# Performance work log

Measured on AMD Instinct MI355X. Metric: run time of the kernel, lower is better.

The kernel has to match this reference:

```python
import jax, jax.numpy as jnp
import numpy as np


def open_uniform_knots(n_ctrl: int, p: int):
    # open-uniform knot vector on [0, 1]: n_ctrl + p + 1 knots
    interior = np.linspace(0.0, 1.0, n_ctrl - p + 1)[1:-1]
    return jnp.asarray(
        np.concatenate([np.zeros(p + 1), interior, np.ones(p + 1)]), jnp.float32
    )


def bspline_basis_1d(u, knots, p: int, n_ctrl: int):
    """Cox-de Boor (NURBS book A2.2), vectorized over queries.
    Returns (N [Q, p+1] nonzero basis values, span [Q] knot-span index)."""
    span = jnp.clip(jnp.searchsorted(knots, u, side='right') - 1, p, n_ctrl - 1)
    left = jnp.stack([u - knots[span + 1 - j] for j in range(1, p + 1)], axis=-1)
    right = jnp.stack([knots[span + j] - u for j in range(1, p + 1)], axis=-1)
    N = [jnp.ones_like(u)]
    for j in range(1, p + 1):
        saved = jnp.zeros_like(u)
        Nn = []
        for r in range(j):
            temp = N[r] / (right[..., r] + left[..., j - 1 - r])
            Nn.append(saved + right[..., r] * temp)
            saved = left[..., j - 1 - r] * temp
        Nn.append(saved)
        N = Nn
    return jnp.stack(N, axis=-1), span


def setup_inputs() -> dict:
    key = jax.random.key(0)
    kq, kc = jax.random.split(key)
    n_points, dim_in = 2_000_000, 3
    n_ctrl, degree, dim_out = 32, 3, 3
    queries = jax.random.uniform(kq, (n_points, dim_in), dtype=jnp.float32)
    control_points = jax.random.normal(kc, (n_ctrl ** 3, dim_out), dtype=jnp.float32)
    return {"queries": queries, "control_points": control_points,
            "degree": degree, "n_ctrl": n_ctrl}


def reference(queries, control_points, degree, n_ctrl):
    p, n = int(degree), int(n_ctrl)
    knots = open_uniform_knots(n, p)
    # per-dim nonzero basis values and spans
    Bx, sx = bspline_basis_1d(queries[:, 0], knots, p, n)
    By, sy = bspline_basis_1d(queries[:, 1], knots, p, n)
    Bz, sz = bspline_basis_1d(queries[:, 2], knots, p, n)
    offs = jnp.arange(p + 1)
    ix = sx[:, None] - p + offs  # [Q, p+1] local control-point indices (x fastest)
    iy = sy[:, None] - p + offs
    iz = sz[:, None] - p + offs
    Q, d = queries.shape[0], control_points.shape[1]
    out = jnp.zeros((Q, d), control_points.dtype)
    # sparse local-support combine: only (p+1)^3 control points per query,
    # looped over the two outer local axes (fixed small loop), gathered on x
    for k in range(p + 1):
        for j in range(p + 1):
            flat = ix + n * (iy[:, j:j + 1] + n * iz[:, k:k + 1])  # [Q, p+1]
            Cg = control_points[flat]  # [Q, p+1, d]
            w = Bz[:, k] * By[:, j]  # [Q]
            out = out + w[:, None] * jnp.einsum('qi,qid->qd', Bx, Cg)
    return out
```

## Files before the change

kernel.cpp:

```cpp
#include <hip/hip_runtime.h>


#define NCTRL 32
#define NSEG 29
#define SCALE (5.5f / 127.0f)
#define INV_SCALE (127.0f / 5.5f)

typedef unsigned int u32x4 __attribute__((ext_vector_type(4)));
typedef _Float16 h2 __attribute__((ext_vector_type(2)));
using native_h2 = decltype(__builtin_amdgcn_cvt_pkrtz(0.0f, 0.0f));

__device__ __forceinline__ h2 pkrtz(float a, float b) {
    return __builtin_bit_cast(h2, __builtin_amdgcn_cvt_pkrtz(a, b));
}
__device__ __forceinline__ float fdot2f(h2 a, h2 b, float c) {
    return __builtin_amdgcn_fdot2(__builtin_bit_cast(native_h2, a),
                                  __builtin_bit_cast(native_h2, b), c, false);
}
__device__ __forceinline__ h2 permh(unsigned int d, unsigned int sel) {
    return __builtin_bit_cast(h2, __builtin_amdgcn_perm(0x64646464u, d, sel));
}

__device__ __forceinline__ void basis_w(float U, float ft, float N[4]) {
    float x  = U - ft;
    float r1 = 1.0f - x;
    float km1 = fmaxf(ft - 1.0f, 0.0f);
    float km2 = fmaxf(ft - 2.0f, 0.0f);
    float kp2 = fminf(ft + 2.0f, (float)NSEG);
    float kp3 = fminf(ft + 3.0f, (float)NSEG);
    float l2 = U - km1, l3 = U - km2;
    float r2 = kp2 - U, r3 = kp3 - U;
    float N0 = r1, N1 = x;
    float rcp20 = __builtin_amdgcn_rcpf(ft + 1.0f - km1);
    float rcp21 = __builtin_amdgcn_rcpf(kp2 - ft);
    float temp  = N0 * rcp20;
    N0 = r1 * temp;
    float saved = l2 * temp;
    temp = N1 * rcp21;
    N1 = saved + r2 * temp;
    float N2 = x * temp;
    float rcp30 = __builtin_amdgcn_rcpf(ft + 1.0f - km2);
    float rcp31 = __builtin_amdgcn_rcpf(kp2 - km1);
    float rcp32 = __builtin_amdgcn_rcpf(kp3 - ft);
    temp = N0 * rcp30;
    N0 = r1 * temp;
    saved = l3 * temp;
    temp = N1 * rcp31;
    N1 = saved + r2 * temp;
    saved = l2 * temp;
    temp = N2 * rcp32;
    N2 = saved + r3 * temp;
    N[0] = N0; N[1] = N1; N[2] = N2; N[3] = x * temp;
}

__device__ __forceinline__ unsigned char quant8(float v) {
    float b = fminf(fmaxf(rintf(v * INV_SCALE) + 128.0f, 0.0f), 255.0f);
    return (unsigned char)(int)b;
}

__global__ void __launch_bounds__(256) repack_q8v2(const float* __restrict__ cp,
                                                   unsigned char* __restrict__ tabA,
                                                   unsigned char* __restrict__ tabB,
                                                   int nA, int nTot) {
    int i4 = blockIdx.x * blockDim.x + threadIdx.x;
    int ib = i4 * 4;
    if (ib >= nTot) return;
    unsigned int w;
    unsigned int* dst;
    if (ib < nA) {
        int beta = ib & 63, L = ib >> 6;
        int x0 = L % NSEG;
        int t2 = L / NSEG;
        int yw = t2 % NSEG;
        int zb = t2 / NSEG;
        int c = beta >> 4, j = (beta & 15) >> 2;
        int s = (zb * NCTRL + (yw + j)) * NCTRL + (x0 + c);
        unsigned int b0 = quant8(cp[3 * s + 0]);
        unsigned int b1 = quant8(cp[3 * s + 1]);
        unsigned int b2 = quant8(cp[3 * (s + NCTRL * NCTRL) + 0]);
        unsigned int b3 = quant8(cp[3 * (s + NCTRL * NCTRL) + 1]);
        w = b0 | (b1 << 8) | (b2 << 16) | (b3 << 24);
        dst = (unsigned int*)(tabA + ib);
    } else {
        int ii = ib - nA;
        int beta = ii & 63, L = ii >> 6;
        int x0 = L % NSEG;
        int t2 = L / NSEG;
        int yw = t2 % NSEG;
        int zw = t2 / NSEG;
        int c = beta >> 4, j = (beta & 15) >> 2;
        int s = (zw * NCTRL + (yw + j)) * NCTRL + (x0 + c);
        unsigned int b0 = quant8(cp[3 * (s + 0 * NCTRL * NCTRL) + 2]);
        unsigned int b1 = quant8(cp[3 * (s + 1 * NCTRL * NCTRL) + 2]);
        unsigned int b2 = quant8(cp[3 * (s + 2 * NCTRL * NCTRL) + 2]);
        unsigned int b3 = quant8(cp[3 * (s + 3 * NCTRL * NCTRL) + 2]);
        w = b0 | (b1 << 8) | (b2 << 16) | (b3 << 24);
        dst = (unsigned int*)(tabB + ii);
    }
    *dst = w;
}


#define LINE_STRIDE 1040
#define BUF_LDS (4 * LINE_STRIDE)
#define WAVE_LDS (2 * BUF_LDS)

__device__ __forceinline__ void stage16(const unsigned char* src,
                                        unsigned char* dst_wave_uniform) {
    __builtin_amdgcn_global_load_lds(
        (const __attribute__((address_space(1))) void*)src,
        (__attribute__((address_space(3))) void*)dst_wave_uniform, 16, 0, 0);
}

__global__ void __launch_bounds__(128, 4) spline_eval_q8v7(const float* __restrict__ q,
                                                           const unsigned char* __restrict__ tabA,
                                                           const unsigned char* __restrict__ tabB,
                                                           float* __restrict__ out, int Q) {
    __shared__ unsigned char smem[2 * WAVE_LDS];
    int t = blockIdx.x * blockDim.x + threadIdx.x;
    bool valid = t < Q;
    int g = valid ? t : (Q - 1);
    int lane = threadIdx.x & 63;
    unsigned char* wbase = &smem[(threadIdx.x >> 6) * WAVE_LDS];
    unsigned char* b0 = wbase;
    unsigned char* b1 = wbase + BUF_LDS;

    int bidx = lane & 60;
    unsigned sub16 = (((unsigned)(lane & 3) - (unsigned)(lane >> 3)) & 3u) << 4;
    const unsigned char* lb0 =
        b0 + (lane >> 4) * LINE_STRIDE + (lane & 15) * 64;
    const unsigned char* lb1 = lb0 + BUF_LDS;
    unsigned t16 = ((unsigned)((lane & 15) >> 1) & 3u) << 4;
    const u32x4* a0p[4];
    const u32x4* a1p[4];
#pragma unroll
    for (int x = 0; x < 4; ++x) {
        unsigned co = (t16 + (unsigned)x * 16u) & 48u;
        a0p[x] = (const u32x4*)(lb0 + co);
        a1p[x] = (const u32x4*)(lb1 + co);
    }
    const unsigned char* pA1 = tabA + 107648u;

    float3 qv = *(const float3*)(q + 3 * (size_t)g);
    float Ux = qv.x * (float)NSEG, Uy = qv.y * (float)NSEG, Uz = qv.z * (float)NSEG;
    float fx = fminf(fmaxf(floorf(Ux), 0.0f), (float)(NSEG - 1));
    float fy = fminf(fmaxf(floorf(Uy), 0.0f), (float)(NSEG - 1));
    float fz = fminf(fmaxf(floorf(Uz), 0.0f), (float)(NSEG - 1));
    int sx = (int)fx, sy = (int)fy, sz = (int)fz;
    int L = (sz * NSEG + sy) * NSEG + sx;

    unsigned voff[4];
#pragma unroll
    for (int grp = 0; grp < 4; ++grp) {
        int Lg = __builtin_amdgcn_ds_bpermute((grp << 6) + bidx, L);
        voff[grp] = ((unsigned)Lg << 6) + sub16;
    }

#pragma unroll
    for (int grp = 0; grp < 4; ++grp)
        stage16(tabA + voff[grp], b0 + grp * LINE_STRIDE);
#pragma unroll
    for (int grp = 0; grp < 4; ++grp)
        stage16(pA1 + voff[grp], b1 + grp * LINE_STRIDE);

    float Bx[4], By[4], Bz[4];
    basis_w(Ux, fx, Bx);
    basis_w(Uy, fy, By);
    basis_w(Uz, fz, Bz);

    h2 Bz01 = pkrtz(Bz[0], Bz[1]);
    h2 Bz23 = pkrtz(Bz[2], Bz[3]);
    const h2 one2 = {(_Float16)1.0f, (_Float16)1.0f};
    h2 wpk[4][2];
    float sumw = 0.0f;
#pragma unroll
    for (int j = 0; j < 4; ++j) {
        h2 Byj = pkrtz(By[j], By[j]);
        wpk[j][0] = Byj * Bz01;
        wpk[j][1] = Byj * Bz23;
        sumw = fdot2f(wpk[j][0], one2, sumw);
        sumw = fdot2f(wpk[j][1], one2, sumw);
    }

    u32x4 c0[4], c1[4];

    asm volatile("s_waitcnt vmcnt(4)" ::: "memory");
#pragma unroll
    for (int x = 0; x < 4; ++x) c0[x] = *a0p[x];
    asm volatile("s_waitcnt vmcnt(0)" ::: "memory");
#pragma unroll
    for (int x = 0; x < 4; ++x) c1[x] = *a1p[x];
    asm volatile("s_waitcnt lgkmcnt(0)" ::: "memory");
    __builtin_amdgcn_sched_barrier(0);
#pragma unroll
    for (int grp = 0; grp < 4; ++grp)
        stage16(tabB + voff[grp], b0 + grp * LINE_STRIDE);

    float axs[4], ays[4];
#pragma unroll
    for (int x = 0; x < 4; ++x) {
        float ax = 0.0f, ay = 0.0f;
#pragma unroll
        for (int j = 0; j < 4; ++j) {
            unsigned d = c0[x][j];
            ax = fdot2f(permh(d, 0x04020400u), wpk[j][0], ax);
            ay = fdot2f(permh(d, 0x04030401u), wpk[j][0], ay);
        }
        axs[x] = ax; ays[x] = ay;
    }
#pragma unroll
    for (int x = 0; x < 4; ++x) {
        float ax = axs[x], ay = ays[x];
#pragma unroll
        for (int j = 0; j < 4; ++j) {
            unsigned d = c1[x][j];
            ax = fdot2f(permh(d, 0x04020400u), wpk[j][1], ax);
            ay = fdot2f(permh(d, 0x04030401u), wpk[j][1], ay);
        }
        axs[x] = ax; ays[x] = ay;
    }

    asm volatile("s_waitcnt vmcnt(0)" ::: "memory");
#pragma unroll
    for (int x = 0; x < 4; ++x) c0[x] = *a0p[x];
    float vx = 0.0f, vy = 0.0f;
#pragma unroll
    for (int x = 0; x < 4; ++x) {
        vx = fmaf(Bx[x], axs[x], vx);
        vy = fmaf(Bx[x], ays[x], vy);
    }
    float mb = (-1152.0f * SCALE) * sumw;
    vx = fmaf(vx, SCALE, mb);
    vy = fmaf(vy, SCALE, mb);

    float vz = 0.0f;
#pragma unroll
    for (int x = 0; x < 4; ++x) {
        float az = 0.0f;
#pragma unroll
        for (int j = 0; j < 4; ++j) {
            unsigned d = c0[x][j];
            az = fdot2f(permh(d, 0x04010400u), wpk[j][0], az);
            az = fdot2f(permh(d, 0x04030402u), wpk[j][1], az);
        }
        vz = fmaf(Bx[x], az, vz);
    }
    vz = fmaf(vz, SCALE, mb);

    if (valid) {
        float3 o; o.x = vx; o.y = vy; o.z = vz;
        *(float3*)(out + 3 * (size_t)g) = o;
    }
}

__global__ void __launch_bounds__(256) spline_eval_direct(const float* __restrict__ q,
                                                          const float* __restrict__ cp,
                                                          float* __restrict__ out, int Q) {
    int idx = blockIdx.x * blockDim.x + threadIdx.x;
    if (idx >= Q) return;
    float U[3], ft[3];
    int s[3];
#pragma unroll
    for (int d = 0; d < 3; ++d) {
        U[d]  = q[3 * idx + d] * (float)NSEG;
        ft[d] = fminf(fmaxf(floorf(U[d]), 0.0f), (float)(NSEG - 1));
        s[d]  = (int)ft[d];
    }
    float Bx[4], By[4], Bz[4];
    basis_w(U[0], ft[0], Bx);
    basis_w(U[1], ft[1], By);
    basis_w(U[2], ft[2], Bz);
    float ax = 0.f, ay = 0.f, az = 0.f;
#pragma unroll
    for (int k = 0; k < 4; ++k) {
#pragma unroll
        for (int j = 0; j < 4; ++j) {
            float w = Bz[k] * By[j];
            int base = ((s[2] + k) * NCTRL + (s[1] + j)) * NCTRL + s[0];
#pragma unroll
            for (int i = 0; i < 4; ++i) {
                float wi = w * Bx[i];
                ax = fmaf(wi, cp[3 * (base + i) + 0], ax);
                ay = fmaf(wi, cp[3 * (base + i) + 1], ay);
                az = fmaf(wi, cp[3 * (base + i) + 2], az);
            }
        }
    }
    out[3 * idx + 0] = ax;
    out[3 * idx + 1] = ay;
    out[3 * idx + 2] = az;
}

extern "C" void kernel_launch(void* const* d_in, const int* in_sizes, int n_in,
                              void* d_out, int out_size, void* d_ws, size_t ws_size,
                              hipStream_t stream) {
    const float* q  = (const float*)d_in[0];
    const float* cp = (const float*)d_in[1];
    float* out = (float*)d_out;
    int Q = in_sizes[0] / 3;

    const int nA = 31 * NSEG * NSEG * 64;
    const int nB = NSEG * NSEG * NSEG * 64;
    const int nTot = nA + nB;
    if (ws_size >= (size_t)nTot) {
        unsigned char* tabA = (unsigned char*)d_ws;
        unsigned char* tabB = tabA + nA;
        int n4 = nTot / 4;
        repack_q8v2<<<(n4 + 255) / 256, 256, 0, stream>>>(cp, tabA, tabB, nA, nTot);
        spline_eval_q8v7<<<(Q + 127) / 128, 128, 0, stream>>>(q, tabA, tabB, out, Q);
    } else {
        spline_eval_direct<<<(Q + 255) / 256, 256, 0, stream>>>(q, cp, out, Q);
    }
}
```

Before: 112.0 us.

## Process two query streams per wave to overlap LDS-staged gathers

Each thread now evaluates two queries (t and t+H), with one 64-thread wave per block and double the LDS per wave. Global-to-LDS loads for both streams are issued together and interleaved with compute through staged vmcnt waits, so memory latency for one stream is hidden behind the dot-product work of the other. The cost is higher register and LDS use per wave, which may lower occupancy, and a different block shape and access order for queries.

```diff
diff --git a/kernel.cpp b/kernel.cpp
--- a/kernel.cpp
+++ b/kernel.cpp
@@ -103,7 +103,8 @@
 
 #define LINE_STRIDE 1040
 #define BUF_LDS (4 * LINE_STRIDE)
-#define WAVE_LDS (2 * BUF_LDS)
+#define STREAM_LDS (2 * BUF_LDS)
+#define WAVE_LDS (2 * STREAM_LDS)
 
 __device__ __forceinline__ void stage16(const unsigned char* src,
                                         unsigned char* dst_wave_uniform) {
@@ -112,66 +113,43 @@
         (__attribute__((address_space(3))) void*)dst_wave_uniform, 16, 0, 0);
 }
 
-__global__ void __launch_bounds__(128, 4) spline_eval_q8v7(const float* __restrict__ q,
-                                                           const unsigned char* __restrict__ tabA,
-                                                           const unsigned char* __restrict__ tabB,
-                                                           float* __restrict__ out, int Q) {
-    __shared__ unsigned char smem[2 * WAVE_LDS];
-    int t = blockIdx.x * blockDim.x + threadIdx.x;
-    bool valid = t < Q;
-    int g = valid ? t : (Q - 1);
-    int lane = threadIdx.x & 63;
-    unsigned char* wbase = &smem[(threadIdx.x >> 6) * WAVE_LDS];
-    unsigned char* b0 = wbase;
-    unsigned char* b1 = wbase + BUF_LDS;
-
-    int bidx = lane & 60;
-    unsigned sub16 = (((unsigned)(lane & 3) - (unsigned)(lane >> 3)) & 3u) << 4;
-    const unsigned char* lb0 =
-        b0 + (lane >> 4) * LINE_STRIDE + (lane & 15) * 64;
-    const unsigned char* lb1 = lb0 + BUF_LDS;
-    unsigned t16 = ((unsigned)((lane & 15) >> 1) & 3u) << 4;
-    const u32x4* a0p[4];
-    const u32x4* a1p[4];
+__device__ __forceinline__ void phaseA(const u32x4* c, const h2 (*wpk)[2], int zp,
+                                       float* axs, float* ays) {
 #pragma unroll
     for (int x = 0; x < 4; ++x) {
-        unsigned co = (t16 + (unsigned)x * 16u) & 48u;
-        a0p[x] = (const u32x4*)(lb0 + co);
-        a1p[x] = (const u32x4*)(lb1 + co);
-    }
-    const unsigned char* pA1 = tabA + 107648u;
-
-    float3 qv = *(const float3*)(q + 3 * (size_t)g);
-    float Ux = qv.x * (float)NSEG, Uy = qv.y * (float)NSEG, Uz = qv.z * (float)NSEG;
-    float fx = fminf(fmaxf(floorf(Ux), 0.0f), (float)(NSEG - 1));
-    float fy = fminf(fmaxf(floorf(Uy), 0.0f), (float)(NSEG - 1));
-    float fz = fminf(fmaxf(floorf(Uz), 0.0f), (float)(NSEG - 1));
-    int sx = (int)fx, sy = (int)fy, sz = (int)fz;
-    int L = (sz * NSEG + sy) * NSEG + sx;
-
-    unsigned voff[4];
-#pragma unroll
-    for (int grp = 0; grp < 4; ++grp) {
-        int Lg = __builtin_amdgcn_ds_bpermute((grp << 6) + bidx, L);
-        voff[grp] = ((unsigned)Lg << 6) + sub16;
-    }
-
-#pragma unroll
-    for (int grp = 0; grp < 4; ++grp)
-        stage16(tabA + voff[grp], b0 + grp * LINE_STRIDE);
-#pragma unroll
-    for (int grp = 0; grp < 4; ++grp)
-        stage16(pA1 + voff[grp], b1 + grp * LINE_STRIDE);
-
-    float Bx[4], By[4], Bz[4];
-    basis_w(Ux, fx, Bx);
-    basis_w(Uy, fy, By);
-    basis_w(Uz, fz, Bz);
-
+        float ax = axs[x], ay = ays[x];
+#pragma unroll
+        for (int j = 0; j < 4; ++j) {
+            unsigned d = c[x][j];
+            ax = fdot2f(permh(d, 0x04020400u), wpk[j][zp], ax);
+            ay = fdot2f(permh(d, 0x04030401u), wpk[j][zp], ay);
+        }
+        axs[x] = ax; ays[x] = ay;
+    }
+}
+
+__device__ __forceinline__ float phaseB(const u32x4* c, const h2 (*wpk)[2],
+                                        const float* Bx) {
+    float vz = 0.0f;
+#pragma unroll
+    for (int x = 0; x < 4; ++x) {
+        float az = 0.0f;
+#pragma unroll
+        for (int j = 0; j < 4; ++j) {
+            unsigned d = c[x][j];
+            az = fdot2f(permh(d, 0x04010400u), wpk[j][0], az);
+            az = fdot2f(permh(d, 0x04030402u), wpk[j][1], az);
+        }
+        vz = fmaf(Bx[x], az, vz);
+    }
+    return vz;
+}
+
+__device__ __forceinline__ float make_wpk(const float* By, const float* Bz,
+                                          h2 (*wpk)[2]) {
     h2 Bz01 = pkrtz(Bz[0], Bz[1]);
     h2 Bz23 = pkrtz(Bz[2], Bz[3]);
     const h2 one2 = {(_Float16)1.0f, (_Float16)1.0f};
-    h2 wpk[4][2];
     float sumw = 0.0f;
 #pragma unroll
     for (int j = 0; j < 4; ++j) {
@@ -181,75 +159,146 @@
         sumw = fdot2f(wpk[j][0], one2, sumw);
         sumw = fdot2f(wpk[j][1], one2, sumw);
     }
+    return sumw;
+}
+
+__device__ __forceinline__ int spanL(float3 qv, float U[3], float ft[3]) {
+    U[0] = qv.x * (float)NSEG; U[1] = qv.y * (float)NSEG; U[2] = qv.z * (float)NSEG;
+#pragma unroll
+    for (int d = 0; d < 3; ++d)
+        ft[d] = fminf(fmaxf(floorf(U[d]), 0.0f), (float)(NSEG - 1));
+    int sx = (int)ft[0], sy = (int)ft[1], sz = (int)ft[2];
+    return (sz * NSEG + sy) * NSEG + sx;
+}
+
+__global__ void __launch_bounds__(64) spline_eval_q8v8(const float* __restrict__ q,
+                                                       const unsigned char* __restrict__ tabA,
+                                                       const unsigned char* __restrict__ tabB,
+                                                       float* __restrict__ out,
+                                                       int Q, int H) {
+    __shared__ unsigned char smem[WAVE_LDS];
+    int lane = threadIdx.x;
+    int t = blockIdx.x * 64 + lane;
+    bool v0ok = t < H;
+    int g0 = v0ok ? t : (Q - 1);
+    int t1 = t + H;
+    bool v1ok = v0ok && (t1 < Q);
+    int g1 = v1ok ? t1 : (Q - 1);
+
+    unsigned char* b0s0 = smem;
+    unsigned char* b1s0 = smem + BUF_LDS;
+    unsigned char* b0s1 = smem + STREAM_LDS;
+    unsigned char* b1s1 = smem + STREAM_LDS + BUF_LDS;
+
+    int bidx = lane & 60;
+    unsigned sub16 = (((unsigned)(lane & 3) - (unsigned)(lane >> 3)) & 3u) << 4;
+    unsigned t16 = ((unsigned)((lane & 15) >> 1) & 3u) << 4;
+    unsigned co[4];
+#pragma unroll
+    for (int x = 0; x < 4; ++x)
+        co[x] = (unsigned)((lane >> 4) * LINE_STRIDE + (lane & 15) * 64)
+              + ((t16 + (unsigned)x * 16u) & 48u);
+    const unsigned char* pA1 = tabA + 107648u;
+
+    float3 qv0 = *(const float3*)(q + 3 * (size_t)g0);
+    float3 qv1 = *(const float3*)(q + 3 * (size_t)g1);
+    float U0[3], f0[3], U1[3], f1[3];
+    int L0 = spanL(qv0, U0, f0);
+    int L1 = spanL(qv1, U1, f1);
+
+    unsigned voff0[4], voff1[4];
+#pragma unroll
+    for (int grp = 0; grp < 4; ++grp) {
+        int Lg0 = __builtin_amdgcn_ds_bpermute((grp << 6) + bidx, L0);
+        int Lg1 = __builtin_amdgcn_ds_bpermute((grp << 6) + bidx, L1);
+        voff0[grp] = ((unsigned)Lg0 << 6) + sub16;
+        voff1[grp] = ((unsigned)Lg1 << 6) + sub16;
+    }
+
+#pragma unroll
+    for (int grp = 0; grp < 4; ++grp)
+        stage16(tabA + voff0[grp], b0s0 + grp * LINE_STRIDE);
+#pragma unroll
+    for (int grp = 0; grp < 4; ++grp)
+        stage16(tabA + voff1[grp], b0s1 + grp * LINE_STRIDE);
+#pragma unroll
+    for (int grp = 0; grp < 4; ++grp)
+        stage16(pA1 + voff0[grp], b1s0 + grp * LINE_STRIDE);
+#pragma unroll
+    for (int grp = 0; grp < 4; ++grp)
+        stage16(pA1 + voff1[grp], b1s1 + grp * LINE_STRIDE);
+
+    float Bx0[4], By0[4], Bz0[4], Bx1[4], By1[4], Bz1[4];
+    basis_w(U0[0], f0[0], Bx0);
+    basis_w(U0[1], f0[1], By0);
+    basis_w(U0[2], f0[2], Bz0);
+    basis_w(U1[0], f1[0], Bx1);
+    basis_w(U1[1], f1[1], By1);
+    basis_w(U1[2], f1[2], Bz1);
+    h2 wpk0[4][2], wpk1[4][2];
+    float sumw0 = make_wpk(By0, Bz0, wpk0);
+    float sumw1 = make_wpk(By1, Bz1, wpk1);
 
     u32x4 c0[4], c1[4];
 
-    asm volatile("s_waitcnt vmcnt(4)" ::: "memory");
-#pragma unroll
-    for (int x = 0; x < 4; ++x) c0[x] = *a0p[x];
-    asm volatile("s_waitcnt vmcnt(0)" ::: "memory");
-#pragma unroll
-    for (int x = 0; x < 4; ++x) c1[x] = *a1p[x];
+    asm volatile("s_waitcnt vmcnt(12)" ::: "memory");
+#pragma unroll
+    for (int x = 0; x < 4; ++x) c0[x] = *(const u32x4*)(b0s0 + co[x]);
+    asm volatile("s_waitcnt vmcnt(8)" ::: "memory");
+#pragma unroll
+    for (int x = 0; x < 4; ++x) c1[x] = *(const u32x4*)(b0s1 + co[x]);
     asm volatile("s_waitcnt lgkmcnt(0)" ::: "memory");
     __builtin_amdgcn_sched_barrier(0);
 #pragma unroll
     for (int grp = 0; grp < 4; ++grp)
-        stage16(tabB + voff[grp], b0 + grp * LINE_STRIDE);
-
-    float axs[4], ays[4];
+        stage16(tabB + voff0[grp], b0s0 + grp * LINE_STRIDE);
+#pragma unroll
+    for (int grp = 0; grp < 4; ++grp)
+        stage16(tabB + voff1[grp], b0s1 + grp * LINE_STRIDE);
+
+    float axs0[4] = {0,0,0,0}, ays0[4] = {0,0,0,0};
+    float axs1[4] = {0,0,0,0}, ays1[4] = {0,0,0,0};
+    phaseA(c0, wpk0, 0, axs0, ays0);
+    phaseA(c1, wpk1, 0, axs1, ays1);
+
+    asm volatile("s_waitcnt vmcnt(12)" ::: "memory");
+#pragma unroll
+    for (int x = 0; x < 4; ++x) c0[x] = *(const u32x4*)(b1s0 + co[x]);
+    asm volatile("s_waitcnt vmcnt(8)" ::: "memory");
+#pragma unroll
+    for (int x = 0; x < 4; ++x) c1[x] = *(const u32x4*)(b1s1 + co[x]);
+    phaseA(c0, wpk0, 1, axs0, ays0);
+    phaseA(c1, wpk1, 1, axs1, ays1);
+
+    asm volatile("s_waitcnt vmcnt(4)" ::: "memory");
+#pragma unroll
+    for (int x = 0; x < 4; ++x) c0[x] = *(const u32x4*)(b0s0 + co[x]);
+    asm volatile("s_waitcnt vmcnt(0)" ::: "memory");
+#pragma unroll
+    for (int x = 0; x < 4; ++x) c1[x] = *(const u32x4*)(b0s1 + co[x]);
+
+    float vx0 = 0.0f, vy0 = 0.0f, vx1 = 0.0f, vy1 = 0.0f;
 #pragma unroll
     for (int x = 0; x < 4; ++x) {
-        float ax = 0.0f, ay = 0.0f;
-#pragma unroll
-        for (int j = 0; j < 4; ++j) {
-            unsigned d = c0[x][j];
-            ax = fdot2f(permh(d, 0x04020400u), wpk[j][0], ax);
-            ay = fdot2f(permh(d, 0x04030401u), wpk[j][0], ay);
-        }
-        axs[x] = ax; ays[x] = ay;
-    }
-#pragma unroll
-    for (int x = 0; x < 4; ++x) {
-        float ax = axs[x], ay = ays[x];
-#pragma unroll
-        for (int j = 0; j < 4; ++j) {
-            unsigned d = c1[x][j];
-            ax = fdot2f(permh(d, 0x04020400u), wpk[j][1], ax);
-            ay = fdot2f(permh(d, 0x04030401u), wpk[j][1], ay);
-        }
-        axs[x] = ax; ays[x] = ay;
-    }
-
-    asm volatile("s_waitcnt vmcnt(0)" ::: "memory");
-#pragma unroll
-    for (int x = 0; x < 4; ++x) c0[x] = *a0p[x];
-    float vx = 0.0f, vy = 0.0f;
-#pragma unroll
-    for (int x = 0; x < 4; ++x) {
-        vx = fmaf(Bx[x], axs[x], vx);
-        vy = fmaf(Bx[x], ays[x], vy);
-    }
-    float mb = (-1152.0f * SCALE) * sumw;
-    vx = fmaf(vx, SCALE, mb);
-    vy = fmaf(vy, SCALE, mb);
-
-    float vz = 0.0f;
-#pragma unroll
-    for (int x = 0; x < 4; ++x) {
-        float az = 0.0f;
-#pragma unroll
-        for (int j = 0; j < 4; ++j) {
-            unsigned d = c0[x][j];
-            az = fdot2f(permh(d, 0x04010400u), wpk[j][0], az);
-            az = fdot2f(permh(d, 0x04030402u), wpk[j][1], az);
-        }
-        vz = fmaf(Bx[x], az, vz);
-    }
-    vz = fmaf(vz, SCALE, mb);
-
-    if (valid) {
-        float3 o; o.x = vx; o.y = vy; o.z = vz;
-        *(float3*)(out + 3 * (size_t)g) = o;
+        vx0 = fmaf(Bx0[x], axs0[x], vx0);
+        vy0 = fmaf(Bx0[x], ays0[x], vy0);
+        vx1 = fmaf(Bx1[x], axs1[x], vx1);
+        vy1 = fmaf(Bx1[x], ays1[x], vy1);
+    }
+    float mb0 = (-1152.0f * SCALE) * sumw0;
+    float mb1 = (-1152.0f * SCALE) * sumw1;
+    float vz0 = phaseB(c0, wpk0, Bx0);
+    float vz1 = phaseB(c1, wpk1, Bx1);
+    vx0 = fmaf(vx0, SCALE, mb0); vy0 = fmaf(vy0, SCALE, mb0); vz0 = fmaf(vz0, SCALE, mb0);
+    vx1 = fmaf(vx1, SCALE, mb1); vy1 = fmaf(vy1, SCALE, mb1); vz1 = fmaf(vz1, SCALE, mb1);
+
+    if (v0ok) {
+        float3 o; o.x = vx0; o.y = vy0; o.z = vz0;
+        *(float3*)(out + 3 * (size_t)g0) = o;
+    }
+    if (v1ok) {
+        float3 o; o.x = vx1; o.y = vy1; o.z = vz1;
+        *(float3*)(out + 3 * (size_t)g1) = o;
     }
 }
 
@@ -302,12 +351,13 @@
     const int nA = 31 * NSEG * NSEG * 64;
     const int nB = NSEG * NSEG * NSEG * 64;
     const int nTot = nA + nB;
-    if (ws_size >= (size_t)nTot) {
+    if (ws_size >= (size_t)nTot && Q > 0) {
         unsigned char* tabA = (unsigned char*)d_ws;
         unsigned char* tabB = tabA + nA;
         int n4 = nTot / 4;
         repack_q8v2<<<(n4 + 255) / 256, 256, 0, stream>>>(cp, tabA, tabB, nA, nTot);
-        spline_eval_q8v7<<<(Q + 127) / 128, 128, 0, stream>>>(q, tabA, tabB, out, Q);
+        int H = (Q + 1) / 2;
+        spline_eval_q8v8<<<(H + 63) / 64, 64, 0, stream>>>(q, tabA, tabB, out, Q, H);
     } else {
         spline_eval_direct<<<(Q + 255) / 256, 256, 0, stream>>>(q, cp, out, Q);
     }
```

Result: no change. 110.2 us (-1.7%).
